# Kernel optimization log

Measured on AMD Instinct MI355X. Metric: run time of the kernel, lower is better.

The kernel has to match this reference:

```python
import jax, jax.numpy as jnp
import numpy as np

DELTA = 1
DROP_DC = False
EPS = 1e-8


def _shell_labels(D, H, W, delta):
    # radial frequency magnitude in cycles/voxel, assuming cubic-ish volume
    fx = jnp.fft.fftfreq(D)[:, None, None]
    fy = jnp.fft.fftfreq(H)[None, :, None]
    fz = jnp.fft.fftfreq(W)[None, None, :]
    r = jnp.sqrt(fx * fx + fy * fy + fz * fz)  # [D,H,W]
    n = min(D, H, W)
    nbins = n // (2 * delta)          # shells up to Nyquist (0.5 cyc/voxel)
    df = delta / n                    # shell width in frequency units
    labels = jnp.minimum((r / df).astype(jnp.int32), nbins)  # overflow bin = nbins
    return labels.reshape(-1), nbins


def setup_inputs() -> dict:
    key = jax.random.key(0)
    k1, k2 = jax.random.split(key)
    shape = (2, 1, 256, 256, 256)
    img_ref = jax.random.normal(k1, shape, dtype=jnp.float32)
    img_pred = jax.random.normal(k2, shape, dtype=jnp.float32)
    return {"img_ref": img_ref, "img_pred": img_pred}


def reference(img_ref, img_pred):
    B, C, D, H, W = img_ref.shape
    labels, nbins = _shell_labels(D, H, W, DELTA)

    F1 = jnp.fft.fftn(img_ref, axes=(-3, -2, -1))   # complex64 [B,C,D,H,W]
    F2 = jnp.fft.fftn(img_pred, axes=(-3, -2, -1))

    cross = jnp.real(F1 * jnp.conj(F2)).reshape(B * C, -1)
    p1 = (jnp.real(F1) ** 2 + jnp.imag(F1) ** 2).reshape(B * C, -1)
    p2 = (jnp.real(F2) ** 2 + jnp.imag(F2) ** 2).reshape(B * C, -1)

    def seg(x):  # radial shell sum; drop the overflow bin beyond Nyquist
        return jax.ops.segment_sum(x, labels, num_segments=nbins + 1)[:nbins]

    num = jax.vmap(seg)(cross)   # [B*C, nbins]
    d1 = jax.vmap(seg)(p1)
    d2 = jax.vmap(seg)(p2)

    fsc = num / jnp.sqrt(d1 * d2 + EPS)
    if DROP_DC:
        fsc = fsc[:, 1:]
    loss = 1.0 - jnp.mean(fsc ** 2)
    return loss
```

## Files before the change

### kernel.cpp

```cpp
#include <hip/hip_runtime.h>
#include <math.h>

#define NDIM 256
#define VOL  (NDIM*NDIM*NDIM)
#define NB   128

__device__ __forceinline__ int br8(int x) { return (int)(__brev((unsigned)x) >> 24); }

__global__ __launch_bounds__(256) void fftz_pack(const float* __restrict__ re_in,
                                                 const float* __restrict__ im_in,
                                                 float2* __restrict__ out)
{
    __shared__ float2 buf[2][4][NDIM];
    __shared__ float2 tw[128];
    const int t = threadIdx.x;
    const int w = t >> 6, lane = t & 63;
    const int L = blockIdx.x * 4 + w;
    const float* rp = re_in + (size_t)L * NDIM;
    const float* ip = im_in + (size_t)L * NDIM;

    if (t < 128) {
        float sn, cs;
        __sincosf(-(float)M_PI * (float)t / 128.0f, &sn, &cs);
        tw[t] = make_float2(cs, sn);
    }
    for (int r = 0; r < 4; ++r) {
        int k = lane + 64 * r;
        buf[0][w][k] = make_float2(rp[k], ip[k]);
    }
    __syncthreads();

    int p = 0;
    for (int st = 0; st < 8; ++st) {
        const int Ns = 1 << st;
        for (int h = 0; h < 2; ++h) {
            int j  = lane + 64 * h;
            int jm = j & (Ns - 1);
            float2 v0 = buf[p][w][j];
            float2 v1 = buf[p][w][j + 128];
            float2 tt = tw[jm << (7 - st)];
            float2 v1r = make_float2(v1.x * tt.x - v1.y * tt.y,
                                     v1.x * tt.y + v1.y * tt.x);
            int idxD = ((j >> st) << (st + 1)) + jm;
            buf[p ^ 1][w][idxD]      = make_float2(v0.x + v1r.x, v0.y + v1r.y);
            buf[p ^ 1][w][idxD + Ns] = make_float2(v0.x - v1r.x, v0.y - v1r.y);
        }
        __syncthreads();
        p ^= 1;
    }

    float2* op = out + (size_t)L * NDIM;
    for (int r = 0; r < 4; ++r) {
        int k = lane + 64 * r;
        op[k] = buf[p][w][k];
    }
}

__global__ __launch_bounds__(256) void fft_strided(float2* __restrict__ A,
                                                   int lineStride, int outerStride)
{
    __shared__ float2 tile[NDIM * 17];
    __shared__ float2 tw[128];
    const int t = threadIdx.x;
    const int l = t & 15, u = t >> 4;
    const int o = blockIdx.x >> 4, c = blockIdx.x & 15;
    const long long base = (long long)o * outerStride + c * 16;

    if (t < 128) {
        float sn, cs;
        __sincosf(-(float)M_PI * (float)t / 128.0f, &sn, &cs);
        tw[t] = make_float2(cs, sn);
    }
    for (int it = 0; it < 16; ++it) {
        int pos = u + it * 16;
        tile[pos * 17 + l] = A[base + (long long)pos * lineStride + l];
    }
    __syncthreads();

    for (int st = 7; st >= 0; --st) {
        const int s = 1 << st;
        for (int it = 0; it < 8; ++it) {
            int m  = u + (it << 4);
            int jm = m & (s - 1);
            int i0 = ((m >> st) << (st + 1)) + jm;
            int i1 = i0 + s;
            float2 a0 = tile[i0 * 17 + l];
            float2 a1 = tile[i1 * 17 + l];
            tile[i0 * 17 + l] = make_float2(a0.x + a1.x, a0.y + a1.y);
            float dx = a0.x - a1.x, dy = a0.y - a1.y;
            float2 tt = tw[jm << (7 - st)];
            tile[i1 * 17 + l] = make_float2(dx * tt.x - dy * tt.y,
                                            dx * tt.y + dy * tt.x);
        }
        __syncthreads();
    }

    for (int it = 0; it < 16; ++it) {
        int pos = u + it * 16;
        A[base + (long long)pos * lineStride + l] = tile[pos * 17 + l];
    }
}

__global__ __launch_bounds__(256) void reduce_shells(const float2* __restrict__ A,
                                                     float* __restrict__ bins)
{
    __shared__ float bs[4][3 * NB];
    const int t = threadIdx.x;
    const int w = t >> 6;
    for (int i = t; i < 4 * 3 * NB; i += 256) ((float*)bs)[i] = 0.f;
    __syncthreads();

    const int pz  = t;
    const int izc = (pz < 128) ? pz : 256 - pz;
    const int iz2 = izc * izc;
    const int pzp = (256 - pz) & 255;

    float2 z1[8], z2[8];
    int   lc2[8];
    float wgt[8];

    #pragma unroll
    for (int jj = 0; jj < 8; ++jj) {
        int L = blockIdx.x * 8 + jj;
        int px = L >> 8, py = L & 255;
        int fx = br8(px), fy = br8(py);
        int fxp = (256 - fx) & 255, fyp = (256 - fy) & 255;
        int Lp = br8(fxp) * 256 + br8(fyp);
        int ax = (fx < 128) ? fx : 256 - fx;
        int ay = (fy < 128) ? fy : 256 - fy;
        int c2 = ax * ax + ay * ay;
        lc2[jj] = -1;
        if (Lp < L) continue;
        if (c2 + 1 > NB * NB) continue;
        lc2[jj] = c2;
        wgt[jj] = (Lp == L) ? 1.f : 2.f;
        z1[jj] = A[(long long)L  * 256 + pz];
        z2[jj] = A[(long long)Lp * 256 + pzp];
    }

    #pragma unroll
    for (int jj = 0; jj < 8; ++jj) {
        if (lc2[jj] < 0) continue;
        int m = lc2[jj] + iz2;
        int lab = (int)sqrtf((float)m);
        if (lab >= NB) continue;
        float2 a = z1[jj], b = z2[jj];
        float F1r = 0.5f * (a.x + b.x);
        float F1i = 0.5f * (a.y - b.y);
        float F2r = 0.5f * (a.y + b.y);
        float F2i = 0.5f * (b.x - a.x);
        float g = wgt[jj];
        atomicAdd(&bs[w][lab],           g * (F1r * F2r + F1i * F2i));
        atomicAdd(&bs[w][NB + lab],      g * (F1r * F1r + F1i * F1i));
        atomicAdd(&bs[w][2 * NB + lab],  g * (F2r * F2r + F2i * F2i));
    }
    __syncthreads();
    for (int i = t; i < 3 * NB; i += 256) {
        float v = bs[0][i] + bs[1][i] + bs[2][i] + bs[3][i];
        if (v != 0.f) atomicAdd(&bins[i], v);
    }
}

__global__ void zero_bins(float* bins)
{
    int t = blockIdx.x * blockDim.x + threadIdx.x;
    if (t < 2 * 3 * NB) bins[t] = 0.f;
}

__global__ void finalize(const float* __restrict__ binsAll, float* __restrict__ out)
{
    __shared__ float red[256];
    const int t = threadIdx.x;
    const int b = t >> 7, bin = t & 127;
    const float* bb = binsAll + b * 3 * NB;
    float num = bb[bin], d1 = bb[NB + bin], d2 = bb[2 * NB + bin];
    float fsc = num / sqrtf(d1 * d2 + 1e-8f);
    red[t] = fsc * fsc;
    __syncthreads();
    for (int s = 128; s > 0; s >>= 1) {
        if (t < s) red[t] += red[t + s];
        __syncthreads();
    }
    if (t == 0) out[0] = 1.f - red[0] / 256.f;
}

__global__ void ws_too_small(float* out) { out[0] = -1.0e9f; }

extern "C" void kernel_launch(void* const* d_in, const int* in_sizes, int n_in,
                              void* d_out, int out_size, void* d_ws, size_t ws_size,
                              hipStream_t stream)
{
    const float* ref  = (const float*)d_in[0];
    const float* pred = (const float*)d_in[1];
    float* out = (float*)d_out;

    const size_t volBytes = (size_t)VOL * sizeof(float2);
    if (ws_size < volBytes + 4096) {
        ws_too_small<<<1, 1, 0, stream>>>(out);
        return;
    }
    float2* A   = (float2*)d_ws;
    float* bins = (float*)((char*)d_ws + volBytes);

    zero_bins<<<1, 1024, 0, stream>>>(bins);

    for (int b = 0; b < 2; ++b) {
        fftz_pack  <<<16384, 256, 0, stream>>>(ref + (size_t)b * VOL,
                                               pred + (size_t)b * VOL, A);
        fft_strided<<<4096, 256, 0, stream>>>(A, 256,   65536);
        fft_strided<<<4096, 256, 0, stream>>>(A, 65536, 256);
        reduce_shells<<<8192, 256, 0, stream>>>(A, bins + b * 3 * NB);
    }
    finalize<<<1, 256, 0, stream>>>(bins, out);
}
```

Measured before the change: 730.1 us.

## Switch 3D FFT passes from radix-2 to radix-4 with vectorized strided loads

After: 668.3 us. -8.5%, faster.

```diff
diff --git a/kernel.cpp b/kernel.cpp
--- a/kernel.cpp
+++ b/kernel.cpp
@@ -5,99 +5,148 @@
 #define VOL  (NDIM*NDIM*NDIM)
 #define NB   128
 
-__device__ __forceinline__ int br8(int x) { return (int)(__brev((unsigned)x) >> 24); }
+__device__ __forceinline__ int dr4(int x) {
+    int b = (int)(__brev((unsigned)x) >> 24);
+    return ((b >> 1) & 0x55) | ((b << 1) & 0xAA);
+}
+__device__ __forceinline__ float2 cmul(float2 a, float2 b) {
+    return make_float2(a.x * b.x - a.y * b.y, a.x * b.y + a.y * b.x);
+}
+__device__ __forceinline__ float2 cadd(float2 a, float2 b){ return make_float2(a.x+b.x, a.y+b.y); }
+__device__ __forceinline__ float2 csub(float2 a, float2 b){ return make_float2(a.x-b.x, a.y-b.y); }
+__device__ __forceinline__ float2 cmuli_neg(float2 a){ return make_float2(a.y, -a.x); }
+__device__ __forceinline__ float2 cmuli_pos(float2 a){ return make_float2(-a.y, a.x); }
 
 __global__ __launch_bounds__(256) void fftz_pack(const float* __restrict__ re_in,
                                                  const float* __restrict__ im_in,
                                                  float2* __restrict__ out)
 {
-    __shared__ float2 buf[2][4][NDIM];
-    __shared__ float2 tw[128];
-    const int t = threadIdx.x;
-    const int w = t >> 6, lane = t & 63;
+    __shared__ float2 buf[4][2][NDIM];
+    const int t = threadIdx.x;
+    const int w = t >> 6, j = t & 63;
     const int L = blockIdx.x * 4 + w;
     const float* rp = re_in + (size_t)L * NDIM;
     const float* ip = im_in + (size_t)L * NDIM;
 
-    if (t < 128) {
+    float2 v0 = make_float2(rp[j      ], ip[j      ]);
+    float2 v1 = make_float2(rp[j +  64], ip[j +  64]);
+    float2 v2 = make_float2(rp[j + 128], ip[j + 128]);
+    float2 v3 = make_float2(rp[j + 192], ip[j + 192]);
+
+    {
+        float2 t0=cadd(v0,v2), t1=csub(v0,v2), t2=cadd(v1,v3), t3=csub(v1,v3);
+        buf[w][0][4*j    ] = cadd(t0, t2);
+        buf[w][0][4*j + 1] = cadd(t1, cmuli_neg(t3));
+        buf[w][0][4*j + 2] = csub(t0, t2);
+        buf[w][0][4*j + 3] = cadd(t1, cmuli_pos(t3));
+    }
+    __builtin_amdgcn_sched_barrier(0);
+
+    int p = 0;
+    #pragma unroll
+    for (int stage = 1; stage <= 2; ++stage) {
+        const int Ns = (stage == 1) ? 4 : 16;
+        const int jm = j & (Ns - 1);
+        float2 a0 = buf[w][p][j      ];
+        float2 a1 = buf[w][p][j +  64];
+        float2 a2 = buf[w][p][j + 128];
+        float2 a3 = buf[w][p][j + 192];
         float sn, cs;
-        __sincosf(-(float)M_PI * (float)t / 128.0f, &sn, &cs);
+        __sincosf(-(float)(2.0 * M_PI) * (float)jm / (float)(4 * Ns), &sn, &cs);
+        float2 w1 = make_float2(cs, sn);
+        float2 w2 = cmul(w1, w1);
+        float2 w3 = cmul(w2, w1);
+        a1 = cmul(a1, w1); a2 = cmul(a2, w2); a3 = cmul(a3, w3);
+        float2 t0=cadd(a0,a2), t1=csub(a0,a2), t2=cadd(a1,a3), t3=csub(a1,a3);
+        const int idxD = (j / Ns) * (4 * Ns) + jm;
+        buf[w][p^1][idxD         ] = cadd(t0, t2);
+        buf[w][p^1][idxD +     Ns] = cadd(t1, cmuli_neg(t3));
+        buf[w][p^1][idxD + 2 * Ns] = csub(t0, t2);
+        buf[w][p^1][idxD + 3 * Ns] = cadd(t1, cmuli_pos(t3));
+        p ^= 1;
+        __builtin_amdgcn_sched_barrier(0);
+    }
+
+    {
+        float2 a0 = buf[w][p][j      ];
+        float2 a1 = buf[w][p][j +  64];
+        float2 a2 = buf[w][p][j + 128];
+        float2 a3 = buf[w][p][j + 192];
+        float sn, cs;
+        __sincosf(-(float)(2.0 * M_PI) * (float)j / 256.0f, &sn, &cs);
+        float2 w1 = make_float2(cs, sn);
+        float2 w2 = cmul(w1, w1);
+        float2 w3 = cmul(w2, w1);
+        a1 = cmul(a1, w1); a2 = cmul(a2, w2); a3 = cmul(a3, w3);
+        float2 t0=cadd(a0,a2), t1=csub(a0,a2), t2=cadd(a1,a3), t3=csub(a1,a3);
+        float2* op = out + (size_t)L * NDIM;
+        op[j      ] = cadd(t0, t2);
+        op[j +  64] = cadd(t1, cmuli_neg(t3));
+        op[j + 128] = csub(t0, t2);
+        op[j + 192] = cadd(t1, cmuli_pos(t3));
+    }
+}
+
+__global__ __launch_bounds__(256) void fft_strided(float2* __restrict__ A,
+                                                   int lineStride, int outerStride)
+{
+    __shared__ float2 tile[NDIM * 18];
+    __shared__ float2 tw[NDIM];
+    const int t = threadIdx.x;
+    {
+        float sn, cs;
+        __sincosf(-(float)(2.0 * M_PI) * (float)t / 256.0f, &sn, &cs);
         tw[t] = make_float2(cs, sn);
     }
-    for (int r = 0; r < 4; ++r) {
-        int k = lane + 64 * r;
-        buf[0][w][k] = make_float2(rp[k], ip[k]);
-    }
-    __syncthreads();
-
-    int p = 0;
-    for (int st = 0; st < 8; ++st) {
-        const int Ns = 1 << st;
-        for (int h = 0; h < 2; ++h) {
-            int j  = lane + 64 * h;
-            int jm = j & (Ns - 1);
-            float2 v0 = buf[p][w][j];
-            float2 v1 = buf[p][w][j + 128];
-            float2 tt = tw[jm << (7 - st)];
-            float2 v1r = make_float2(v1.x * tt.x - v1.y * tt.y,
-                                     v1.x * tt.y + v1.y * tt.x);
-            int idxD = ((j >> st) << (st + 1)) + jm;
-            buf[p ^ 1][w][idxD]      = make_float2(v0.x + v1r.x, v0.y + v1r.y);
-            buf[p ^ 1][w][idxD + Ns] = make_float2(v0.x - v1r.x, v0.y - v1r.y);
+    const int l4 = t & 7, u8 = t >> 3;
+    const int o = blockIdx.x >> 4, c = blockIdx.x & 15;
+    const long long base = (long long)o * outerStride + c * 16;
+
+    #pragma unroll
+    for (int it = 0; it < 8; ++it) {
+        int pos = u8 + it * 32;
+        const float4 d = *(const float4*)&A[base + (long long)pos * lineStride + 2 * l4];
+        tile[pos * 18 + 2 * l4    ] = make_float2(d.x, d.y);
+        tile[pos * 18 + 2 * l4 + 1] = make_float2(d.z, d.w);
+    }
+    __syncthreads();
+
+    const int l = t & 15, u = t >> 4;
+    #pragma unroll
+    for (int ls = 6; ls >= 0; ls -= 2) {
+        const int s = 1 << ls;
+        #pragma unroll
+        for (int it = 0; it < 4; ++it) {
+            int m  = u + it * 16;
+            int jm = m & (s - 1);
+            int bidx = ((m >> ls) << (ls + 2)) + jm;
+            float2 a  = tile[(bidx        ) * 18 + l];
+            float2 b  = tile[(bidx +     s) * 18 + l];
+            float2 cc = tile[(bidx + 2 * s) * 18 + l];
+            float2 d  = tile[(bidx + 3 * s) * 18 + l];
+            float2 t0=cadd(a,cc), t1=csub(a,cc), t2=cadd(b,d), t3=csub(b,d);
+            float2 y0 = cadd(t0, t2);
+            float2 y1 = cadd(t1, cmuli_neg(t3));
+            float2 y2 = csub(t0, t2);
+            float2 y3 = cadd(t1, cmuli_pos(t3));
+            int k1 = jm << (6 - ls);
+            y1 = cmul(y1, tw[k1]);
+            y2 = cmul(y2, tw[2 * k1]);
+            y3 = cmul(y3, tw[3 * k1]);
+            tile[(bidx        ) * 18 + l] = y0;
+            tile[(bidx +     s) * 18 + l] = y1;
+            tile[(bidx + 2 * s) * 18 + l] = y2;
+            tile[(bidx + 3 * s) * 18 + l] = y3;
         }
         __syncthreads();
-        p ^= 1;
-    }
-
-    float2* op = out + (size_t)L * NDIM;
-    for (int r = 0; r < 4; ++r) {
-        int k = lane + 64 * r;
-        op[k] = buf[p][w][k];
-    }
-}
-
-__global__ __launch_bounds__(256) void fft_strided(float2* __restrict__ A,
-                                                   int lineStride, int outerStride)
-{
-    __shared__ float2 tile[NDIM * 17];
-    __shared__ float2 tw[128];
-    const int t = threadIdx.x;
-    const int l = t & 15, u = t >> 4;
-    const int o = blockIdx.x >> 4, c = blockIdx.x & 15;
-    const long long base = (long long)o * outerStride + c * 16;
-
-    if (t < 128) {
-        float sn, cs;
-        __sincosf(-(float)M_PI * (float)t / 128.0f, &sn, &cs);
-        tw[t] = make_float2(cs, sn);
-    }
-    for (int it = 0; it < 16; ++it) {
-        int pos = u + it * 16;
-        tile[pos * 17 + l] = A[base + (long long)pos * lineStride + l];
-    }
-    __syncthreads();
-
-    for (int st = 7; st >= 0; --st) {
-        const int s = 1 << st;
-        for (int it = 0; it < 8; ++it) {
-            int m  = u + (it << 4);
-            int jm = m & (s - 1);
-            int i0 = ((m >> st) << (st + 1)) + jm;
-            int i1 = i0 + s;
-            float2 a0 = tile[i0 * 17 + l];
-            float2 a1 = tile[i1 * 17 + l];
-            tile[i0 * 17 + l] = make_float2(a0.x + a1.x, a0.y + a1.y);
-            float dx = a0.x - a1.x, dy = a0.y - a1.y;
-            float2 tt = tw[jm << (7 - st)];
-            tile[i1 * 17 + l] = make_float2(dx * tt.x - dy * tt.y,
-                                            dx * tt.y + dy * tt.x);
-        }
-        __syncthreads();
-    }
-
-    for (int it = 0; it < 16; ++it) {
-        int pos = u + it * 16;
-        A[base + (long long)pos * lineStride + l] = tile[pos * 17 + l];
+    }
+
+    #pragma unroll
+    for (int it = 0; it < 8; ++it) {
+        int pos = u8 + it * 32;
+        float2 e0 = tile[pos * 18 + 2 * l4], e1 = tile[pos * 18 + 2 * l4 + 1];
+        *(float4*)&A[base + (long long)pos * lineStride + 2 * l4] =
+            make_float4(e0.x, e0.y, e1.x, e1.y);
     }
 }
 
@@ -123,15 +172,15 @@
     for (int jj = 0; jj < 8; ++jj) {
         int L = blockIdx.x * 8 + jj;
         int px = L >> 8, py = L & 255;
-        int fx = br8(px), fy = br8(py);
+        int fx = dr4(px), fy = dr4(py);
         int fxp = (256 - fx) & 255, fyp = (256 - fy) & 255;
-        int Lp = br8(fxp) * 256 + br8(fyp);
+        int Lp = dr4(fxp) * 256 + dr4(fyp);
         int ax = (fx < 128) ? fx : 256 - fx;
         int ay = (fy < 128) ? fy : 256 - fy;
         int c2 = ax * ax + ay * ay;
         lc2[jj] = -1;
         if (Lp < L) continue;
-        if (c2 + 1 > NB * NB) continue;
+        if (c2 >= NB * NB) continue;
         lc2[jj] = c2;
         wgt[jj] = (Lp == L) ? 1.f : 2.f;
         z1[jj] = A[(long long)L  * 256 + pz];
```
